# Kernel optimization log

Hardware: AMD Instinct MI355X
Metric: run time of the kernel (lower is better)

Reference implementation:

```python
import jax, jax.numpy as jnp
import numpy as np

B, LQ, LKV, E, H, D, P = 2, 2048, 2048, 1024, 16, 64, 64
NEG = -1e10


def setup_inputs() -> dict:
    key = jax.random.key(0)
    ks = jax.random.split(key, 8)
    inputs_q = jax.random.normal(ks[0], (B, LQ, E), jnp.float32)
    inputs_kv = jax.random.normal(ks[1], (B, LKV, E), jnp.float32)
    key_prefix = jax.random.normal(ks[2], (B, P, H, D), jnp.float32)
    value_prefix = jax.random.normal(ks[3], (B, P, H, D), jnp.float32)
    # causal mask, broadcastable over heads: [B, 1, LQ, LKV]
    mask = jnp.broadcast_to(jnp.tril(jnp.ones((LQ, LKV), bool)), (B, 1, LQ, LKV))
    scale = 1.0 / np.sqrt(E)  # fan_in variance scaling
    Wq = jax.random.normal(ks[4], (E, H, D), jnp.float32) * scale
    Wk = jax.random.normal(ks[5], (E, H, D), jnp.float32) * scale
    Wv = jax.random.normal(ks[6], (E, H, D), jnp.float32) * scale
    Wo = jax.random.normal(ks[7], (H, D, E), jnp.float32) * (1.0 / np.sqrt(H * D))
    return dict(inputs_q=inputs_q, inputs_kv=inputs_kv, key_prefix=key_prefix,
                value_prefix=value_prefix, mask=mask, Wq=Wq, Wk=Wk, Wv=Wv, Wo=Wo)


def reference(inputs_q, inputs_kv, key_prefix, value_prefix, mask, Wq, Wk, Wv, Wo):
    depth_scaling = jnp.sqrt(jnp.asarray(D, inputs_q.dtype))
    # query kernel is divided by sqrt(head_dim) at init -> fold into projection
    q = jnp.einsum('bqe,ehd->bqhd', inputs_q, Wq) / depth_scaling
    k = jnp.einsum('bke,ehd->bkhd', inputs_kv, Wk)
    v = jnp.einsum('bke,ehd->bkhd', inputs_kv, Wv)
    # prefix concat on the key/value length axis
    k = jnp.concatenate([key_prefix, k], axis=1)   # [B, P+LKV, H, D]
    v = jnp.concatenate([value_prefix, v], axis=1)
    # mask -> additive bias; prefix tokens get zero bias (always attendable)
    bias = jnp.where(mask, 0.0, NEG).astype(inputs_q.dtype)      # [B,1,LQ,LKV]
    prefix_bias = jnp.zeros(bias.shape[:-1] + (P,), bias.dtype)  # [B,1,LQ,P]
    bias = jnp.concatenate([prefix_bias, bias], axis=-1)         # [B,1,LQ,P+LKV]
    scores = jnp.einsum('bqhd,bkhd->bhqk', q, k) + bias
    probs = jax.nn.softmax(scores, axis=-1)
    ctx = jnp.einsum('bhqk,bkhd->bqhd', probs, v)
    return jnp.einsum('bqhd,hde->bqe', ctx, Wo)
```

## Files before the change

### kernel.cpp

```cpp
#include <hip/hip_runtime.h>
#include <hip/hip_bf16.h>

#define B_   2
#define LQ_  2048
#define LKV_ 2048
#define E_   1024
#define H_   16
#define D_   64
#define P_   64
#define LT_  (P_ + LKV_)
#define NEG_ -1e10f
#define LOG2E_ 1.4426950408889634f

typedef unsigned short ushort_t;
typedef unsigned int   uint_t;
typedef float f32x4   __attribute__((ext_vector_type(4)));
typedef float f32x16  __attribute__((ext_vector_type(16)));
typedef short bf16x8  __attribute__((ext_vector_type(8)));
typedef uint_t u32x4  __attribute__((ext_vector_type(4)));

__device__ __forceinline__ ushort_t f2bf(float f) {
    union { float f; uint_t u; } v; v.f = f;
    return (ushort_t)((v.u + 0x7fffu + ((v.u >> 16) & 1u)) >> 16);
}

__device__ __forceinline__ uint_t cvt_pk_bf16(float lo, float hi) {
    uint_t r;
    asm("v_cvt_pk_bf16_f32 %0, %1, %2" : "=v"(r) : "v"(lo), "v"(hi));
    return r;
}

__device__ __forceinline__ float exp2x(float x) {
    float r;
    asm("v_exp_f32 %0, %1" : "=v"(r) : "v"(x));
    return r;
}

__device__ __forceinline__ float bflo(uint_t u) {
    return __builtin_bit_cast(float, u << 16);
}
__device__ __forceinline__ float bfhi(uint_t u) {
    return __builtin_bit_cast(float, u & 0xFFFF0000u);
}


#define GLOAD16(gp, lp)                                                     \
    __builtin_amdgcn_global_load_lds(                                       \
        (const __attribute__((address_space(1))) void*)(gp),                \
        (__attribute__((address_space(3))) void*)(lp), 16, 0, 0)

__global__ __launch_bounds__(256) void prep(
    const float* __restrict__ iq, const float* __restrict__ ikv,
    const float* __restrict__ w0, const float* __restrict__ w1,
    const float* __restrict__ w2, const float* __restrict__ w3,
    const float* __restrict__ kp, const float* __restrict__ vp,
    ushort_t* __restrict__ Aq, ushort_t* __restrict__ Akv,
    ushort_t* __restrict__ d0, ushort_t* __restrict__ d1,
    ushort_t* __restrict__ d2, ushort_t* __restrict__ d3,
    ushort_t* __restrict__ kws, ushort_t* __restrict__ vws)
{
    __shared__ float t[32][33];
    const int blk = blockIdx.x;
    const int tid = threadIdx.x;

    if (blk < 8192) {
        const int idx = blk * 256 + tid;
        constexpr int HALF = 4096 * 1024 / 4;
        const float4 v = (idx < HALF) ? ((const float4*)iq)[idx]
                                      : ((const float4*)ikv)[idx - HALF];
        const uint2 p = make_uint2((uint_t)f2bf(v.x) | ((uint_t)f2bf(v.y) << 16),
                                   (uint_t)f2bf(v.z) | ((uint_t)f2bf(v.w) << 16));
        if (idx < HALF) ((uint2*)Aq)[idx] = p;
        else            ((uint2*)Akv)[idx - HALF] = p;
    } else if (blk < 12288) {
        const int tr = blk - 8192;
        const int bz = tr >> 10, rem = tr & 1023;
        const int x0 = (rem & 31) * 32, y0 = (rem >> 5) * 32;
        const float* S = (bz == 0) ? w0 : (bz == 1) ? w1 : (bz == 2) ? w2 : w3;
        ushort_t* D = (bz == 0) ? d0 : (bz == 1) ? d1 : (bz == 2) ? d2 : d3;
        const int tx = tid & 31, ty = tid >> 5;
        #pragma unroll
        for (int i = 0; i < 4; ++i)
            t[ty + i * 8][tx] = S[(size_t)(y0 + ty + i * 8) * 1024 + x0 + tx];
        __syncthreads();
        #pragma unroll
        for (int i = 0; i < 4; ++i)
            D[(size_t)(x0 + ty + i * 8) * 1024 + (y0 + tx)] =
                f2bf(t[tx][ty + i * 8]);
    } else {
        const int idx = (blk - 12288) * 256 + tid;
        const int d4 = idx & 15;
        const int h  = (idx >> 4) & 15;
        const int p  = (idx >> 8) & 63;
        const int b  = idx >> 14;
        const float4 kv = ((const float4*)kp)[idx];
        const float4 vv = ((const float4*)vp)[idx];
        const size_t kdst = ((size_t)(b * H_ + h) * LT_ + p) * D_ + d4 * 4;
        *(uint2*)(kws + kdst) =
            make_uint2((uint_t)f2bf(kv.x) | ((uint_t)f2bf(kv.y) << 16),
                       (uint_t)f2bf(kv.z) | ((uint_t)f2bf(kv.w) << 16));
        const float* vs = (const float*)&vv;
        #pragma unroll
        for (int i = 0; i < 4; ++i)
            vws[((size_t)(b * H_ + h) * D_ + d4 * 4 + i) * LT_ + p] = f2bf(vs[i]);
    }
}

__device__ __forceinline__ void gemm_core(const ushort_t* __restrict__ A,
                                          const ushort_t* __restrict__ Wt,
                                          ushort_t* As, ushort_t* Bs,
                                          int m0, int n0, f32x4 (*acc)[4])
{
    constexpr int K = 1024, NSTEP = 16;
    const int tid  = threadIdx.x;
    const int lane = tid & 63;
    const int wave = tid >> 6;
    const int l15 = lane & 15, lg = lane >> 4;
    const int wr = (wave >> 1) * 32;
    const int wc = (wave & 1) * 64;
    const uint_t xr = (uint_t)((l15 & 7) << 4);

    for (int i = 0; i < NSTEP; ++i) {
        const int k0 = i * 64;
        #pragma unroll
        for (int j = 0; j < 2; ++j) {
            const int c = j * 256 + tid;
            const int row = c >> 3, cc = c & 7;
            const size_t so = (size_t)row * K + k0 + ((cc ^ (row & 7)) * 8);
            GLOAD16(A + (size_t)m0 * K + so, (char*)As + (j * 256 + wave * 64) * 16);
        }
        #pragma unroll
        for (int j = 0; j < 4; ++j) {
            const int c = j * 256 + tid;
            const int row = c >> 3, cc = c & 7;
            const size_t so = (size_t)row * K + k0 + ((cc ^ (row & 7)) * 8);
            GLOAD16(Wt + (size_t)n0 * K + so, (char*)Bs + (j * 256 + wave * 64) * 16);
        }
        asm volatile("s_waitcnt vmcnt(0)" ::: "memory");
        __builtin_amdgcn_s_barrier();

        bf16x8 af[2][2], bfr[2][4];
        #pragma unroll
        for (int kt = 0; kt < 2; ++kt) {
            #pragma unroll
            for (int mt = 0; mt < 2; ++mt)
                af[kt][mt] = *(const bf16x8*)((const char*)As + (wr + mt * 16 + l15) * 128
                                              + ((kt * 64 + lg * 16) ^ xr));
            #pragma unroll
            for (int nt = 0; nt < 4; ++nt)
                bfr[kt][nt] = *(const bf16x8*)((const char*)Bs + (wc + nt * 16 + l15) * 128
                                               + ((kt * 64 + lg * 16) ^ xr));
        }
        #pragma unroll
        for (int mt = 0; mt < 2; ++mt)
            #pragma unroll
            for (int nt = 0; nt < 4; ++nt) {
                acc[mt][nt] = __builtin_amdgcn_mfma_f32_16x16x32_bf16(
                    af[0][mt], bfr[0][nt], acc[mt][nt], 0, 0, 0);
                acc[mt][nt] = __builtin_amdgcn_mfma_f32_16x16x32_bf16(
                    af[1][mt], bfr[1][nt], acc[mt][nt], 0, 0, 0);
            }

        __builtin_amdgcn_s_barrier();
    }
}

__global__ __launch_bounds__(256) void gemm_qkv(
    const ushort_t* __restrict__ Aq, const ushort_t* __restrict__ Akv,
    const ushort_t* __restrict__ WqT, const ushort_t* __restrict__ WkT,
    const ushort_t* __restrict__ WvT,
    ushort_t* __restrict__ qws, ushort_t* __restrict__ kws,
    ushort_t* __restrict__ vws)
{
    __shared__ __align__(16) ushort_t As[64 * 64];
    __shared__ __align__(16) ushort_t Bs[128 * 64];
    const int by = blockIdx.y, sel = by >> 3;
    const ushort_t* A  = sel ? Akv : Aq;
    const ushort_t* Wt = (sel == 0) ? WqT : (sel == 1) ? WkT : WvT;
    const float scale  = sel ? 1.0f : 0.125f * LOG2E_;
    const int m0 = blockIdx.x * 64, n0 = (by & 7) * 128;

    f32x4 acc[2][4];
    #pragma unroll
    for (int mt = 0; mt < 2; ++mt)
        #pragma unroll
        for (int nt = 0; nt < 4; ++nt) acc[mt][nt] = (f32x4)0.f;

    gemm_core(A, Wt, As, Bs, m0, n0, acc);

    const int lane = threadIdx.x & 63, wave = threadIdx.x >> 6;
    const int l15 = lane & 15, lg = lane >> 4;
    const int wr = (wave >> 1) * 32, wc = (wave & 1) * 64;

    if (sel == 2) {
        #pragma unroll
        for (int mt = 0; mt < 2; ++mt)
            #pragma unroll
            for (int nt = 0; nt < 4; ++nt) {
                const int n = n0 + wc + nt * 16 + l15;
                const int h = n >> 6, d = n & 63;
                const int m = m0 + wr + mt * 16 + lg * 4;
                const int bb = m >> 11, ll = m & 2047;
                const uint2 pk = make_uint2(
                    (uint_t)f2bf(acc[mt][nt][0]) | ((uint_t)f2bf(acc[mt][nt][1]) << 16),
                    (uint_t)f2bf(acc[mt][nt][2]) | ((uint_t)f2bf(acc[mt][nt][3]) << 16));
                *(uint2*)(vws + ((size_t)(bb * H_ + h) * D_ + d) * LT_ + P_ + ll) = pk;
            }
    } else {
        ushort_t* Cw     = (sel == 0) ? qws : kws;
        const int Lout   = (sel == 0) ? LQ_ : LT_;
        const int rowoff = (sel == 0) ? 0 : P_;
        #pragma unroll
        for (int mt = 0; mt < 2; ++mt)
            #pragma unroll
            for (int nt = 0; nt < 4; ++nt) {
                const int n = n0 + wc + nt * 16 + l15;
                const int h = n >> 6, d = n & 63;
                #pragma unroll
                for (int r = 0; r < 4; ++r) {
                    const int m = m0 + wr + mt * 16 + lg * 4 + r;
                    const int bb = m >> 11, ll = m & 2047;
                    Cw[(((size_t)(bb * H_ + h) * Lout) + (rowoff + ll)) * D_ + d] =
                        f2bf(acc[mt][nt][r] * scale);
                }
            }
    }
}

__global__ __launch_bounds__(256) void gemm_out(const ushort_t* __restrict__ A,
                                                const ushort_t* __restrict__ Wt,
                                                float* __restrict__ C)
{
    __shared__ __align__(16) ushort_t As[64 * 64];
    __shared__ __align__(16) ushort_t Bs[128 * 64];
    const int m0 = blockIdx.x * 64, n0 = blockIdx.y * 128;

    f32x4 acc[2][4];
    #pragma unroll
    for (int mt = 0; mt < 2; ++mt)
        #pragma unroll
        for (int nt = 0; nt < 4; ++nt) acc[mt][nt] = (f32x4)0.f;

    gemm_core(A, Wt, As, Bs, m0, n0, acc);

    const int lane = threadIdx.x & 63, wave = threadIdx.x >> 6;
    const int l15 = lane & 15, lg = lane >> 4;
    const int wr = (wave >> 1) * 32, wc = (wave & 1) * 64;
    #pragma unroll
    for (int mt = 0; mt < 2; ++mt)
        #pragma unroll
        for (int nt = 0; nt < 4; ++nt) {
            const int n = n0 + wc + nt * 16 + l15;
            #pragma unroll
            for (int r = 0; r < 4; ++r) {
                const int m = m0 + wr + mt * 16 + lg * 4 + r;
                C[(size_t)m * 1024 + n] = acc[mt][nt][r];
            }
        }
}

__global__ __launch_bounds__(256) void attn_mfma(const ushort_t* __restrict__ qws,
                                                 const ushort_t* __restrict__ kws,
                                                 const ushort_t* __restrict__ vws,
                                                 ushort_t* __restrict__ pO,
                                                 float* __restrict__ ml)
{
    const int tid  = threadIdx.x;
    const int lane = tid & 63;
    const int wave = tid >> 6;
    const int z    = blockIdx.x;
    const int slot = z >> 8;
    const int c    = z & 255;
    const int g    = c >> 5;
    const int bh   = c & 31;
    const int seg  = slot >> 1;
    const int qb   = (slot & 1) ? g : (15 - g);

    const ushort_t* Qg  = qws + (size_t)bh * LQ_ * D_;
    const ushort_t* Kg  = kws + (size_t)bh * LT_ * D_;
    const ushort_t* Vtg = vws + (size_t)bh * D_ * LT_;

    __shared__ __align__(16) ushort_t Ks[2 * 64 * 64];
    __shared__ __align__(16) ushort_t Vt[2 * 64 * 64];

    const int l31 = lane & 31;
    const int hi  = lane >> 5;
    const uint_t xsw = (uint_t)((l31 & 7) << 4);
    const int qbase = qb * 128 + wave * 32;
    const int q     = qbase + l31;
    const int qe    = qbase + 31;

    bf16x8 qf[4];
    #pragma unroll
    for (int kd = 0; kd < 4; ++kd)
        qf[kd] = *(const bf16x8*)(Qg + (size_t)q * D_ + kd * 16 + hi * 8);

    f32x16 acc[2];
    acc[0] = (f32x16)0.f;
    acc[1] = (f32x16)0.f;
    float lpreg = 0.f;

    const int ntile = 2 * qb + 3;
    const int i0    = seg ? (qb + 2) : 0;
    const int iend  = seg ? ntile : (qb + 2);

    auto STAGE = [&](int t, int par) {
        const int t0s = t * 64;
        char* kd = (char*)Ks + par * 8192;
        char* vd = (char*)Vt + par * 8192;
        #pragma unroll
        for (int i = 0; i < 2; ++i) {
            const int c2 = i * 256 + tid;
            const int rr = c2 >> 3, cc = c2 & 7;
            GLOAD16(Kg + (size_t)(t0s + rr) * D_ + ((cc ^ (rr & 7)) * 8),
                    kd + (i * 256 + wave * 64) * 16);
            GLOAD16(Vtg + (size_t)rr * LT_ + t0s + ((cc ^ (rr & 7)) * 8),
                    vd + (i * 256 + wave * 64) * 16);
        }
    };

    STAGE(i0, 0);
    STAGE(i0 + 1, 1);

    for (int i = i0; i < iend; ++i) {
        const int t0 = i * 64;
        const int cur = (i - i0) & 1;
        if (i + 1 < iend) {
            asm volatile("s_waitcnt vmcnt(4)" ::: "memory");
        } else {
            asm volatile("s_waitcnt vmcnt(0)" ::: "memory");
        }
        __builtin_amdgcn_s_barrier();

        if (t0 <= P_ + qe) {
            const char* KsB = (const char*)Ks + cur * 8192;
            const char* VtB = (const char*)Vt + cur * 8192;

            f32x16 sv[2];
            __builtin_amdgcn_s_setprio(1);
            #pragma unroll
            for (int th = 0; th < 2; ++th) {
                f32x16 zf = (f32x16)0.f;
                #pragma unroll
                for (int kd = 0; kd < 4; ++kd) {
                    const bf16x8 a = *(const bf16x8*)(
                        KsB + (th * 32 + l31) * 128 + ((kd * 32 + hi * 16) ^ xsw));
                    zf = __builtin_amdgcn_mfma_f32_32x32x16_bf16(a, qf[kd], zf, 0, 0, 0);
                }
                sv[th] = zf;
            }
            __builtin_amdgcn_s_setprio(0);

            if (t0 + 63 > P_ + qbase) {
                #pragma unroll
                for (int th = 0; th < 2; ++th)
                    #pragma unroll
                    for (int r = 0; r < 16; ++r) {
                        const int t = t0 + th * 32 + (r & 3) + 8 * (r >> 2) + 4 * hi;
                        if (!(t < P_ || (t - P_) <= q)) sv[th][r] += NEG_;
                    }
            }

            float rs = 0.f;
            #pragma unroll
            for (int th = 0; th < 2; ++th)
                #pragma unroll
                for (int r = 0; r < 16; ++r) {
                    const float e = exp2x(sv[th][r]);
                    sv[th][r] = e;
                    rs += e;
                }
            lpreg += rs;

            bf16x8 pb[4];
            #pragma unroll
            for (int kt = 0; kt < 4; ++kt) {
                const int th = kt >> 1, base = (kt & 1) * 8;
                uint4 w;
                w.x = cvt_pk_bf16(sv[th][base + 0], sv[th][base + 1]);
                w.y = cvt_pk_bf16(sv[th][base + 2], sv[th][base + 3]);
                w.z = cvt_pk_bf16(sv[th][base + 4], sv[th][base + 5]);
                w.w = cvt_pk_bf16(sv[th][base + 6], sv[th][base + 7]);
                pb[kt] = __builtin_bit_cast(bf16x8, w);
            }

            __builtin_amdgcn_s_setprio(1);
            #pragma unroll
            for (int dh = 0; dh < 2; ++dh) {
                const char* rowp = VtB + (dh * 32 + l31) * 128 + 8 * hi;
                #pragma unroll
                for (int kt = 0; kt < 4; ++kt) {
                    const uint_t off = ((uint_t)(kt * 32)) ^ xsw;
                    const uint2 va = *(const uint2*)(rowp + off);
                    const uint2 vb = *(const uint2*)(rowp + (off ^ 16));
                    uint4 w;
                    w.x = va.x; w.y = va.y; w.z = vb.x; w.w = vb.y;
                    const bf16x8 vfr = __builtin_bit_cast(bf16x8, w);
                    acc[dh] = __builtin_amdgcn_mfma_f32_32x32x16_bf16(
                        vfr, pb[kt], acc[dh], 0, 0, 0);
                }
            }
            __builtin_amdgcn_s_setprio(0);
        }

        __builtin_amdgcn_s_barrier();
        if (i + 2 < iend) STAGE(i + 2, cur);
    }

    const float ltot = lpreg + __shfl_xor(lpreg, 32);
    const size_t qrow = (size_t)(seg * 32 + bh) * 2048 + q;
    #pragma unroll
    for (int dh = 0; dh < 2; ++dh)
        #pragma unroll
        for (int gg = 0; gg < 4; ++gg) {
            const int d = dh * 32 + gg * 8 + hi * 4;
            const uint2 pk = make_uint2(
                cvt_pk_bf16(acc[dh][4 * gg + 0], acc[dh][4 * gg + 1]),
                cvt_pk_bf16(acc[dh][4 * gg + 2], acc[dh][4 * gg + 3]));
            *(uint2*)(pO + qrow * 64 + d) = pk;
        }
    if (hi == 0)
        ml[qrow] = ltot;
}

__global__ __launch_bounds__(256) void attn_merge(const ushort_t* __restrict__ pO,
                                                  const float* __restrict__ ml,
                                                  ushort_t* __restrict__ ctx)
{
    const int idx = blockIdx.x * 256 + threadIdx.x;
    const int dg = idx & 15;
    const int q  = (idx >> 4) & 2047;
    const int bh = idx >> 15;
    const int b = bh >> 4, h = bh & 15;

    const size_t q0 = (size_t)bh * 2048 + q;
    const size_t q1 = (size_t)(32 + bh) * 2048 + q;
    const float inv = 1.0f / (ml[q0] + ml[q1]);

    const uint2 a0 = *(const uint2*)(pO + q0 * 64 + dg * 4);
    const uint2 a1 = *(const uint2*)(pO + q1 * 64 + dg * 4);
    const float o0 = (bflo(a0.x) + bflo(a1.x)) * inv;
    const float o1 = (bfhi(a0.x) + bfhi(a1.x)) * inv;
    const float o2 = (bflo(a0.y) + bflo(a1.y)) * inv;
    const float o3 = (bfhi(a0.y) + bfhi(a1.y)) * inv;

    const uint2 pk = make_uint2(
        (uint_t)f2bf(o0) | ((uint_t)f2bf(o1) << 16),
        (uint_t)f2bf(o2) | ((uint_t)f2bf(o3) << 16));
    *(uint2*)(ctx + (((size_t)b * LQ_ + q) * H_ + h) * D_ + dg * 4) = pk;
}

extern "C" void kernel_launch(void* const* d_in, const int* in_sizes, int n_in,
                              void* d_out, int out_size, void* d_ws, size_t ws_size,
                              hipStream_t stream)
{
    const float* inputs_q     = (const float*)d_in[0];
    const float* inputs_kv    = (const float*)d_in[1];
    const float* key_prefix   = (const float*)d_in[2];
    const float* value_prefix = (const float*)d_in[3];
    const float* Wq = (const float*)d_in[5];
    const float* Wk = (const float*)d_in[6];
    const float* Wv = (const float*)d_in[7];
    const float* Wo = (const float*)d_in[8];
    float* out = (float*)d_out;

    ushort_t* Aq  = (ushort_t*)d_ws;
    ushort_t* Akv = Aq  + (size_t)4096 * 1024;
    ushort_t* WqT = Akv + (size_t)4096 * 1024;
    ushort_t* WkT = WqT + (size_t)1024 * 1024;
    ushort_t* WvT = WkT + (size_t)1024 * 1024;
    ushort_t* WoT = WvT + (size_t)1024 * 1024;
    ushort_t* qws = WoT + (size_t)1024 * 1024;
    ushort_t* kws = qws + (size_t)B_ * H_ * LQ_ * D_;
    ushort_t* vws = kws + (size_t)B_ * H_ * LT_ * D_;
    ushort_t* ctx = vws + (size_t)B_ * H_ * LT_ * D_;

    ushort_t* pO    = Aq;
    float*    mlbuf = (float*)WqT;

    prep<<<12416, 256, 0, stream>>>(inputs_q, inputs_kv, Wq, Wk, Wv, Wo,
                                    key_prefix, value_prefix,
                                    Aq, Akv, WqT, WkT, WvT, WoT, kws, vws);
    gemm_qkv<<<dim3(64, 24), 256, 0, stream>>>(Aq, Akv, WqT, WkT, WvT,
                                               qws, kws, vws);
    attn_mfma<<<2 * B_ * H_ * (LQ_ / 128), 256, 0, stream>>>(qws, kws, vws,
                                                             pO, mlbuf);
    attn_merge<<<4096, 256, 0, stream>>>(pO, mlbuf, ctx);
    gemm_out<<<dim3(64, 8), 256, 0, stream>>>(ctx, WoT, out);
}
```

Measured before the change: 118.1 us.

## Fuse split-KV attention merge into output projection GEMM A-tile load

Removes the separate attn_merge kernel and the ctx buffer. The output GEMM now reads both partial attention outputs and their softmax denominators directly, normalises and sums them, converts to bf16 and writes the A tile into shared memory. This saves one launch plus a write and reread of the ctx tensor. In exchange, the merge is recomputed for each of the 8 column blocks, and the A-tile path becomes synchronous register loads instead of async global-to-LDS copies.

```diff
diff --git a/kernel.cpp b/kernel.cpp
--- a/kernel.cpp
+++ b/kernel.cpp
@@ -227,13 +227,23 @@
     }
 }
 
-__global__ __launch_bounds__(256) void gemm_out(const ushort_t* __restrict__ A,
+__global__ __launch_bounds__(256) void gemm_out(const ushort_t* __restrict__ pO,
+                                                const float* __restrict__ ml,
                                                 const ushort_t* __restrict__ Wt,
                                                 float* __restrict__ C)
 {
+    constexpr int K = 1024, NSTEP = 16;
     __shared__ __align__(16) ushort_t As[64 * 64];
     __shared__ __align__(16) ushort_t Bs[128 * 64];
     const int m0 = blockIdx.x * 64, n0 = blockIdx.y * 128;
+    const int tid  = threadIdx.x;
+    const int lane = tid & 63;
+    const int wave = tid >> 6;
+    const int l15 = lane & 15, lg = lane >> 4;
+    const int wr = (wave >> 1) * 32, wc = (wave & 1) * 64;
+    const uint_t xr = (uint_t)((l15 & 7) << 4);
+    const int bb = m0 >> 11;
+    const int qq0 = m0 & 2047;
 
     f32x4 acc[2][4];
     #pragma unroll
@@ -241,11 +251,64 @@
         #pragma unroll
         for (int nt = 0; nt < 4; ++nt) acc[mt][nt] = (f32x4)0.f;
 
-    gemm_core(A, Wt, As, Bs, m0, n0, acc);
-
-    const int lane = threadIdx.x & 63, wave = threadIdx.x >> 6;
-    const int l15 = lane & 15, lg = lane >> 4;
-    const int wr = (wave >> 1) * 32, wc = (wave & 1) * 64;
+    for (int i = 0; i < NSTEP; ++i) {
+        const int k0 = i * 64;
+        #pragma unroll
+        for (int j = 0; j < 2; ++j) {
+            const int c = j * 256 + tid;
+            const int row = c >> 3, cc = c & 7;
+            const int qq = qq0 + row;
+            const size_t r0 = ((size_t)(bb * 16 + i) * 2048 + qq);
+            const size_t base = r0 * 64 + ((cc ^ (row & 7)) * 8);
+            const uint4 a0 = *(const uint4*)(pO + base);
+            const uint4 a1 = *(const uint4*)(pO + base + (size_t)32 * 2048 * 64);
+            const float inv = 1.0f / (ml[r0] + ml[r0 + 32 * 2048]);
+            uint4 w;
+            w.x = cvt_pk_bf16((bflo(a0.x) + bflo(a1.x)) * inv,
+                              (bfhi(a0.x) + bfhi(a1.x)) * inv);
+            w.y = cvt_pk_bf16((bflo(a0.y) + bflo(a1.y)) * inv,
+                              (bfhi(a0.y) + bfhi(a1.y)) * inv);
+            w.z = cvt_pk_bf16((bflo(a0.z) + bflo(a1.z)) * inv,
+                              (bfhi(a0.z) + bfhi(a1.z)) * inv);
+            w.w = cvt_pk_bf16((bflo(a0.w) + bflo(a1.w)) * inv,
+                              (bfhi(a0.w) + bfhi(a1.w)) * inv);
+            *(uint4*)((char*)As + c * 16) = w;
+        }
+        #pragma unroll
+        for (int j = 0; j < 4; ++j) {
+            const int c = j * 256 + tid;
+            const int row = c >> 3, cc = c & 7;
+            const size_t so = (size_t)row * K + k0 + ((cc ^ (row & 7)) * 8);
+            GLOAD16(Wt + (size_t)n0 * K + so, (char*)Bs + (j * 256 + wave * 64) * 16);
+        }
+        asm volatile("s_waitcnt vmcnt(0) lgkmcnt(0)" ::: "memory");
+        __builtin_amdgcn_s_barrier();
+
+        bf16x8 af[2][2], bfr[2][4];
+        #pragma unroll
+        for (int kt = 0; kt < 2; ++kt) {
+            #pragma unroll
+            for (int mt = 0; mt < 2; ++mt)
+                af[kt][mt] = *(const bf16x8*)((const char*)As + (wr + mt * 16 + l15) * 128
+                                              + ((kt * 64 + lg * 16) ^ xr));
+            #pragma unroll
+            for (int nt = 0; nt < 4; ++nt)
+                bfr[kt][nt] = *(const bf16x8*)((const char*)Bs + (wc + nt * 16 + l15) * 128
+                                               + ((kt * 64 + lg * 16) ^ xr));
+        }
+        #pragma unroll
+        for (int mt = 0; mt < 2; ++mt)
+            #pragma unroll
+            for (int nt = 0; nt < 4; ++nt) {
+                acc[mt][nt] = __builtin_amdgcn_mfma_f32_16x16x32_bf16(
+                    af[0][mt], bfr[0][nt], acc[mt][nt], 0, 0, 0);
+                acc[mt][nt] = __builtin_amdgcn_mfma_f32_16x16x32_bf16(
+                    af[1][mt], bfr[1][nt], acc[mt][nt], 0, 0, 0);
+            }
+
+        __builtin_amdgcn_s_barrier();
+    }
+
     #pragma unroll
     for (int mt = 0; mt < 2; ++mt)
         #pragma unroll
@@ -423,33 +486,6 @@
         ml[qrow] = ltot;
 }
 
-__global__ __launch_bounds__(256) void attn_merge(const ushort_t* __restrict__ pO,
-                                                  const float* __restrict__ ml,
-                                                  ushort_t* __restrict__ ctx)
-{
-    const int idx = blockIdx.x * 256 + threadIdx.x;
-    const int dg = idx & 15;
-    const int q  = (idx >> 4) & 2047;
-    const int bh = idx >> 15;
-    const int b = bh >> 4, h = bh & 15;
-
-    const size_t q0 = (size_t)bh * 2048 + q;
-    const size_t q1 = (size_t)(32 + bh) * 2048 + q;
-    const float inv = 1.0f / (ml[q0] + ml[q1]);
-
-    const uint2 a0 = *(const uint2*)(pO + q0 * 64 + dg * 4);
-    const uint2 a1 = *(const uint2*)(pO + q1 * 64 + dg * 4);
-    const float o0 = (bflo(a0.x) + bflo(a1.x)) * inv;
-    const float o1 = (bfhi(a0.x) + bfhi(a1.x)) * inv;
-    const float o2 = (bflo(a0.y) + bflo(a1.y)) * inv;
-    const float o3 = (bfhi(a0.y) + bfhi(a1.y)) * inv;
-
-    const uint2 pk = make_uint2(
-        (uint_t)f2bf(o0) | ((uint_t)f2bf(o1) << 16),
-        (uint_t)f2bf(o2) | ((uint_t)f2bf(o3) << 16));
-    *(uint2*)(ctx + (((size_t)b * LQ_ + q) * H_ + h) * D_ + dg * 4) = pk;
-}
-
 extern "C" void kernel_launch(void* const* d_in, const int* in_sizes, int n_in,
                               void* d_out, int out_size, void* d_ws, size_t ws_size,
                               hipStream_t stream)
@@ -473,7 +509,6 @@
     ushort_t* qws = WoT + (size_t)1024 * 1024;
     ushort_t* kws = qws + (size_t)B_ * H_ * LQ_ * D_;
     ushort_t* vws = kws + (size_t)B_ * H_ * LT_ * D_;
-    ushort_t* ctx = vws + (size_t)B_ * H_ * LT_ * D_;
 
     ushort_t* pO    = Aq;
     float*    mlbuf = (float*)WqT;
@@ -485,6 +520,5 @@
                                                qws, kws, vws);
     attn_mfma<<<2 * B_ * H_ * (LQ_ / 128), 256, 0, stream>>>(qws, kws, vws,
                                                              pO, mlbuf);
-    attn_merge<<<4096, 256, 0, stream>>>(pO, mlbuf, ctx);
-    gemm_out<<<dim3(64, 8), 256, 0, stream>>>(ctx, WoT, out);
-}
+    gemm_out<<<dim3(64, 8), 256, 0, stream>>>(pO, mlbuf, WoT, out);
+}
```

After: 120.6 us. 1.02x slower.
